# Optimization experiments

Measured on AMD Instinct MI355X. Metric: run time of the kernel, lower is better.

## Reference

```python
import jax, jax.numpy as jnp
import numpy as np
import math

B, S, D, H, L = 4, 2048, 512, 8, 2
HD = D // H
NG = (3, 4, 5)
V = 30000          # n_gram_vocab_size
BASE = 31          # rolling hash base
NPATCH = 16
PLEN = S // NPATCH


def _ln(x, w, b, eps):
    m = x.mean(-1, keepdims=True)
    v = ((x - m) ** 2).mean(-1, keepdims=True)
    return (x - m) * jax.lax.rsqrt(v + eps) * w + b


def setup_inputs() -> dict:
    key = jax.random.key(0)
    ks = jax.random.split(key, 16)

    def nrm(i, shape, std=0.02):
        return jax.random.normal(ks[i], shape, dtype=jnp.float32) * std

    return {
        "byte_seq": jax.random.randint(ks[0], (B, S), 0, 256, dtype=jnp.int32),
        "patch_boundaries": jnp.arange(NPATCH + 1, dtype=jnp.int32) * PLEN,
        "byte_emb": nrm(1, (256, D), 1.0 / math.sqrt(D)),
        "ng_emb": nrm(2, (len(NG), V, D)),
        "tl_qkv_w": nrm(3, (L, 3 * D, D)),
        "tl_qkv_b": jnp.zeros((L, 3 * D), jnp.float32),
        "tl_out_w": nrm(4, (L, D, D)),
        "tl_out_b": jnp.zeros((L, D), jnp.float32),
        "tl_ln1_w": jnp.ones((L, D), jnp.float32),
        "tl_ln1_b": jnp.zeros((L, D), jnp.float32),
        "tl_ln2_w": jnp.ones((L, D), jnp.float32),
        "tl_ln2_b": jnp.zeros((L, D), jnp.float32),
        "tl_ff1_w": nrm(5, (L, 4 * D, D)),
        "tl_ff1_b": jnp.zeros((L, 4 * D), jnp.float32),
        "tl_ff2_w": nrm(6, (L, D, 4 * D)),
        "tl_ff2_b": jnp.zeros((L, D), jnp.float32),
        "ca_qkv_w": nrm(7, (3 * D, D)),
        "ca_qkv_b": jnp.zeros((3 * D,), jnp.float32),
        "ca_out_w": nrm(8, (D, D)),
        "ca_out_b": jnp.zeros((D,), jnp.float32),
        "ca_ln_w": jnp.ones((D,), jnp.float32),
        "ca_ln_b": jnp.zeros((D,), jnp.float32),
        "norm_w": jnp.ones((D,), jnp.float32),
        "norm_b": jnp.zeros((D,), jnp.float32),
    }


def _forward(byte_seq, patch_boundaries, byte_emb, ng_emb,
             tl_qkv_w, tl_qkv_b, tl_out_w, tl_out_b,
             tl_ln1_w, tl_ln1_b, tl_ln2_w, tl_ln2_b,
             tl_ff1_w, tl_ff1_b, tl_ff2_w, tl_ff2_b,
             ca_qkv_w, ca_qkv_b, ca_out_w, ca_out_b, ca_ln_w, ca_ln_b,
             norm_w, norm_b):
    x = byte_emb[byte_seq]                                  # [B,S,D]

    # n-gram rolling hash == polynomial hash mod V; computed in parallel
    # as windowed dot products with modular base powers (exact same values
    # as the sequential rolling-update loop in the torch code).
    ng_scale = 1.0 / (len(NG) + 1)
    for idx, n in enumerate(NG):
        powers = jnp.array([pow(BASE, n - 1 - i, V) for i in range(n)],
                           dtype=byte_seq.dtype)
        windows = jnp.stack([byte_seq[:, j:S - n + 1 + j] for j in range(n)],
                            axis=-1)                        # [B,S-n+1,n]
        h = (windows * powers).sum(-1) % V                   # [B,S-n+1]
        x = x.at[:, n - 1:].add(ng_emb[idx][h] * ng_scale)

    scale = 1.0 / math.sqrt(HD)
    neg = jnp.where(jnp.triu(jnp.ones((S, S), dtype=bool), 1),
                    -jnp.inf, 0.0).astype(x.dtype)           # causal additive mask

    # post-norm TransformerEncoderLayer (relu activation, dropout=0/eval)
    for l in range(L):
        qkv = x @ tl_qkv_w[l].T + tl_qkv_b[l]                # [B,S,3D]
        q, k, v = jnp.split(qkv, 3, axis=-1)
        q = q.reshape(B, S, H, HD).transpose(0, 2, 1, 3)
        k = k.reshape(B, S, H, HD).transpose(0, 2, 1, 3)
        v = v.reshape(B, S, H, HD).transpose(0, 2, 1, 3)
        scores = jnp.einsum('bhqd,bhkd->bhqk', q, k) * scale + neg
        a = jax.nn.softmax(scores, axis=-1)
        o = jnp.einsum('bhqk,bhkd->bhqd', a, v).transpose(0, 2, 1, 3).reshape(B, S, D)
        o = o @ tl_out_w[l].T + tl_out_b[l]
        x = _ln(x + o, tl_ln1_w[l], tl_ln1_b[l], 1e-5)
        ff = jax.nn.relu(x @ tl_ff1_w[l].T + tl_ff1_b[l]) @ tl_ff2_w[l].T + tl_ff2_b[l]
        x = _ln(x + ff, tl_ln2_w[l], tl_ln2_b[l], 1e-5)

    # uniform patch boundaries -> vectorized patch cross-attention
    npatch = patch_boundaries.shape[0] - 1
    plen = S // npatch
    xp = x.reshape(B, npatch, plen, D)
    query = xp.mean(axis=2)                                  # [B,P,D]
    qn = _ln(query, ca_ln_w, ca_ln_b, 1e-6)
    kvn = _ln(xp, ca_ln_w, ca_ln_b, 1e-6)
    wq, wk, wv = jnp.split(ca_qkv_w, 3, axis=0)
    bq, bk, bv = jnp.split(ca_qkv_b, 3)
    q = (qn @ wq.T + bq).reshape(B, npatch, H, HD)
    k = (kvn @ wk.T + bk).reshape(B, npatch, plen, H, HD)
    v = (kvn @ wv.T + bv).reshape(B, npatch, plen, H, HD)
    s = jnp.einsum('bphd,bplhd->bphl', q, k) * scale
    a = jax.nn.softmax(s, axis=-1)
    o = jnp.einsum('bphl,bplhd->bphd', a, v).reshape(B, npatch, D)
    patches = query + (o @ ca_out_w.T + ca_out_b)

    return _ln(x, norm_w, norm_b, 1e-6), _ln(patches, norm_w, norm_b, 1e-6)


def reference(byte_seq, patch_boundaries, byte_emb, ng_emb,
              tl_qkv_w, tl_qkv_b, tl_out_w, tl_out_b,
              tl_ln1_w, tl_ln1_b, tl_ln2_w, tl_ln2_b,
              tl_ff1_w, tl_ff1_b, tl_ff2_w, tl_ff2_b,
              ca_qkv_w, ca_qkv_b, ca_out_w, ca_out_b, ca_ln_w, ca_ln_b,
              norm_w, norm_b):
    return _forward(byte_seq, patch_boundaries, byte_emb, ng_emb,
                    tl_qkv_w, tl_qkv_b, tl_out_w, tl_out_b,
                    tl_ln1_w, tl_ln1_b, tl_ln2_w, tl_ln2_b,
                    tl_ff1_w, tl_ff1_b, tl_ff2_w, tl_ff2_b,
                    ca_qkv_w, ca_qkv_b, ca_out_w, ca_out_b, ca_ln_w, ca_ln_b,
                    norm_w, norm_b)
```

## Files before the change

### kernel.cpp

```cpp
#include <hip/hip_runtime.h>
#include <hip/hip_bf16.h>

#define B_ 4
#define S_ 2048
#define D_ 512
#define H_ 8
#define HD_ 64
#define L_ 2
#define V_ 30000
#define NPATCH_ 16
#define PLEN_ 128

typedef short bf16x8 __attribute__((ext_vector_type(8)));
typedef float f32x4 __attribute__((ext_vector_type(4)));

__device__ __forceinline__ unsigned short f2bf(float f) {
    unsigned u = __float_as_uint(f);
    return (unsigned short)((u + 0x7FFFu + ((u >> 16) & 1u)) >> 16);
}

#define C0_ (2*1536*512/4)
#define C1_ (2*512*512/4)
#define C2_ (2*2048*512/4)
#define C3_ (2*512*2048/4)
#define C4_ (1024*512/4)
__global__ __launch_bounds__(256) void cast5_kernel(
    const float* __restrict__ s0, const float* __restrict__ s1,
    const float* __restrict__ s2, const float* __restrict__ s3,
    const float* __restrict__ s4,
    unsigned short* __restrict__ d0, unsigned short* __restrict__ d1,
    unsigned short* __restrict__ d2, unsigned short* __restrict__ d3,
    unsigned short* __restrict__ d4)
{
    int i = blockIdx.x * 256 + threadIdx.x;
    const float* s; unsigned short* d;
    if      (i < C0_)                  { s = s0; d = d0; }
    else if ((i -= C0_) < C1_)         { s = s1; d = d1; }
    else if ((i -= C1_) < C2_)         { s = s2; d = d2; }
    else if ((i -= C2_) < C3_)         { s = s3; d = d3; }
    else if ((i -= C3_) < C4_)         { s = s4; d = d4; }
    else return;
    const float4 v = *reinterpret_cast<const float4*>(s + (size_t)i * 4);
    ushort4 o;
    o.x = f2bf(v.x); o.y = f2bf(v.y); o.z = f2bf(v.z); o.w = f2bf(v.w);
    *reinterpret_cast<ushort4*>(d + (size_t)i * 4) = o;
}

__global__ __launch_bounds__(128) void embed_ngram_kernel(
    const int* __restrict__ bytes, const float* __restrict__ byte_emb,
    const float* __restrict__ ng_emb, float* __restrict__ x,
    unsigned short* __restrict__ xb)
{
    const int bs = blockIdx.x;
    const int s  = bs % S_;
    const int b  = bs / S_;
    const int d  = threadIdx.x * 4;
    const int* brow = bytes + (size_t)b * S_;

    const int c = brow[s];
    float4 v = *reinterpret_cast<const float4*>(byte_emb + (size_t)c * D_ + d);

    if (s >= 2) {
        int h = (brow[s-2]*961 + brow[s-1]*31 + brow[s]) % V_;
        const float4 g = *reinterpret_cast<const float4*>(ng_emb + ((size_t)0*V_ + h)*D_ + d);
        v.x += 0.25f*g.x; v.y += 0.25f*g.y; v.z += 0.25f*g.z; v.w += 0.25f*g.w;
    }
    if (s >= 3) {
        int h = (brow[s-3]*29791 + brow[s-2]*961 + brow[s-1]*31 + brow[s]) % V_;
        const float4 g = *reinterpret_cast<const float4*>(ng_emb + ((size_t)1*V_ + h)*D_ + d);
        v.x += 0.25f*g.x; v.y += 0.25f*g.y; v.z += 0.25f*g.z; v.w += 0.25f*g.w;
    }
    if (s >= 4) {
        int h = (brow[s-4]*23521 + brow[s-3]*29791 + brow[s-2]*961 + brow[s-1]*31 + brow[s]) % V_;
        const float4 g = *reinterpret_cast<const float4*>(ng_emb + ((size_t)2*V_ + h)*D_ + d);
        v.x += 0.25f*g.x; v.y += 0.25f*g.y; v.z += 0.25f*g.z; v.w += 0.25f*g.w;
    }
    *reinterpret_cast<float4*>(x + (size_t)bs * D_ + d) = v;
    ushort4 o;
    o.x = f2bf(v.x); o.y = f2bf(v.y); o.z = f2bf(v.z); o.w = f2bf(v.w);
    *reinterpret_cast<ushort4*>(xb + (size_t)bs * D_ + d) = o;
}

template<int DO_RELU, int BF16OUT, int BN>
__global__ __launch_bounds__(256) void mgemm_kernel(
    const unsigned short* __restrict__ Xb, const unsigned short* __restrict__ Wb,
    const float* __restrict__ bias, void* __restrict__ Yout,
    int M, int N, int K)
{
    constexpr int NT  = BN / 32;
    constexpr int NLB = BN / 32;
    __shared__ unsigned short As[128*64];
    __shared__ unsigned short Bs[BN*64];

    const int t    = threadIdx.x;
    const int lane = t & 63;
    const int w    = t >> 6;

    const int nwg = gridDim.x * gridDim.y;
    const int bid = blockIdx.y * gridDim.x + blockIdx.x;
    const int swz = (bid & 7) * (nwg >> 3) + (bid >> 3);
    const int bx  = swz % gridDim.x, by = swz / gridDim.x;

    const int bm   = by * 128, bn = bx * BN;
    const int l15  = lane & 15, lg = lane >> 4;
    const int wr   = w >> 1, wc = w & 1;

    int srow[4], scol[4];
#pragma unroll
    for (int i = 0; i < 4; ++i) {
        const int off = w*1024 + i*4096 + lane*16;
        srow[i] = off >> 7;
        scol[i] = ((off >> 4) & 7) ^ (srow[i] & 7);
    }

    f32x4 acc[4][NT];
#pragma unroll
    for (int mt = 0; mt < 4; ++mt)
#pragma unroll
        for (int nt = 0; nt < NT; ++nt) acc[mt][nt] = (f32x4){0.f,0.f,0.f,0.f};

    for (int kt = 0; kt < K; kt += 64) {
#pragma unroll
        for (int i = 0; i < 4; ++i) {
            const unsigned short* gA = Xb + (size_t)(bm + srow[i]) * K + kt + scol[i]*8;
            __builtin_amdgcn_global_load_lds(
                (const __attribute__((address_space(1))) void*)gA,
                (__attribute__((address_space(3))) void*)&As[w*512 + i*2048], 16, 0, 0);
        }
#pragma unroll
        for (int i = 0; i < NLB; ++i) {
            const unsigned short* gB = Wb + (size_t)(bn + srow[i]) * K + kt + scol[i]*8;
            __builtin_amdgcn_global_load_lds(
                (const __attribute__((address_space(1))) void*)gB,
                (__attribute__((address_space(3))) void*)&Bs[w*512 + i*2048], 16, 0, 0);
        }
        __syncthreads();

#pragma unroll
        for (int ks = 0; ks < 2; ++ks) {
            const int c16 = (ks*4 + lg) ^ (l15 & 7);
            bf16x8 a[4], b[NT];
#pragma unroll
            for (int mt = 0; mt < 4; ++mt)
                a[mt] = *reinterpret_cast<const bf16x8*>(&As[(wr*64 + mt*16 + l15)*64 + c16*8]);
#pragma unroll
            for (int nt = 0; nt < NT; ++nt)
                b[nt] = *reinterpret_cast<const bf16x8*>(&Bs[(wc*(BN/2) + nt*16 + l15)*64 + c16*8]);
#pragma unroll
            for (int mt = 0; mt < 4; ++mt)
#pragma unroll
                for (int nt = 0; nt < NT; ++nt)
                    acc[mt][nt] = __builtin_amdgcn_mfma_f32_16x16x32_bf16(
                        a[mt], b[nt], acc[mt][nt], 0, 0, 0);
        }
        __syncthreads();
    }

    float bv[NT];
#pragma unroll
    for (int nt = 0; nt < NT; ++nt) bv[nt] = bias[bn + wc*(BN/2) + nt*16 + l15];

#pragma unroll
    for (int mt = 0; mt < 4; ++mt) {
#pragma unroll
        for (int nt = 0; nt < NT; ++nt) {
            const int n = bn + wc*(BN/2) + nt*16 + l15;
#pragma unroll
            for (int r = 0; r < 4; ++r) {
                const int m = bm + wr*64 + mt*16 + 4*lg + r;
                float v = acc[mt][nt][r] + bv[nt];
                if (DO_RELU) v = fmaxf(v, 0.f);
                if (BF16OUT)
                    ((unsigned short*)Yout)[(size_t)m * N + n] = f2bf(v);
                else
                    ((float*)Yout)[(size_t)m * N + n] = v;
            }
        }
    }
}

__global__ __launch_bounds__(256) void attn_mfma_kernel(
    const unsigned short* __restrict__ qkvb, unsigned short* __restrict__ ob)
{
    __shared__ unsigned short Ks[128*72];
    __shared__ unsigned short Vt[64*136];
    __shared__ unsigned short Plds[4*16*136];

    const int t    = threadIdx.x;
    const int lane = t & 63;
    const int w    = t >> 6;
    const int qp   = blockIdx.x;
    const int bh   = blockIdx.y;
    const int h    = bh & 7;
    const int b    = bh >> 3;

    const unsigned short* base = qkvb + (size_t)b * S_ * 1536;
    const int l15 = lane & 15, lg = lane >> 4;
    const int skey = t >> 1;
    const int sd0  = (t & 1) * 32;
    const int scs  = (((skey >> 3) ^ ((t & 1) << 1)) << 3) + (skey & 7);
    unsigned short* pw_base = Plds + w*16*136;

    bf16x8 kr0, kr1, kr2, kr3, vr0, vr1, vr2, vr3;
#define LOADREG(KT) { \
        const unsigned short* p_ = base + (size_t)((KT) + skey) * 1536 + 512 + h*64 + sd0; \
        kr0 = *reinterpret_cast<const bf16x8*>(p_);       \
        kr1 = *reinterpret_cast<const bf16x8*>(p_ + 8);   \
        kr2 = *reinterpret_cast<const bf16x8*>(p_ + 16);  \
        kr3 = *reinterpret_cast<const bf16x8*>(p_ + 24);  \
        vr0 = *reinterpret_cast<const bf16x8*>(p_ + 512); \
        vr1 = *reinterpret_cast<const bf16x8*>(p_ + 520); \
        vr2 = *reinterpret_cast<const bf16x8*>(p_ + 528); \
        vr3 = *reinterpret_cast<const bf16x8*>(p_ + 536); }

    LOADREG(0);

#pragma unroll
    for (int half = 0; half < 2; ++half) {
        const int qb  = half ? (31 - qp) : qp;
        const int q0w = qb * 64 + w * 16;

        bf16x8 qf0, qf1;
        {
            const unsigned short* qr = base + (size_t)(q0w + l15) * 1536 + h*64 + lg*8;
            qf0 = *reinterpret_cast<const bf16x8*>(qr);
            qf1 = *reinterpret_cast<const bf16x8*>(qr + 32);
        }

        f32x4 oacc[4];
#pragma unroll
        for (int i = 0; i < 4; ++i) oacc[i] = (f32x4){0.f,0.f,0.f,0.f};
        float mrow[4] = {-INFINITY,-INFINITY,-INFINITY,-INFINITY};
        float lrow[4] = {0.f,0.f,0.f,0.f};

        const int ntiles = (qb + 2) >> 1;
        for (int tile = 0; tile < ntiles; ++tile) {
            const int kt = tile * 128;
            __syncthreads();
            *reinterpret_cast<bf16x8*>(&Ks[skey*72 + sd0])      = kr0;
            *reinterpret_cast<bf16x8*>(&Ks[skey*72 + sd0 + 8])  = kr1;
            *reinterpret_cast<bf16x8*>(&Ks[skey*72 + sd0 + 16]) = kr2;
            *reinterpret_cast<bf16x8*>(&Ks[skey*72 + sd0 + 24]) = kr3;
#pragma unroll
            for (int j = 0; j < 8; ++j) Vt[(sd0+j)*136    + scs] = (unsigned short)vr0[j];
#pragma unroll
            for (int j = 0; j < 8; ++j) Vt[(sd0+8+j)*136  + scs] = (unsigned short)vr1[j];
#pragma unroll
            for (int j = 0; j < 8; ++j) Vt[(sd0+16+j)*136 + scs] = (unsigned short)vr2[j];
#pragma unroll
            for (int j = 0; j < 8; ++j) Vt[(sd0+24+j)*136 + scs] = (unsigned short)vr3[j];
            __syncthreads();
            const int nkt = (tile + 1 < ntiles) ? (kt + 128) : 0;
            LOADREG(nkt);

            f32x4 sacc[8];
            __builtin_amdgcn_s_setprio(1);
#pragma unroll
            for (int kt16 = 0; kt16 < 8; ++kt16) {
                sacc[kt16] = (f32x4){0.f,0.f,0.f,0.f};
                const unsigned short* kp = &Ks[(kt16*16 + l15)*72 + lg*8];
                bf16x8 k0 = *reinterpret_cast<const bf16x8*>(kp);
                bf16x8 k1 = *reinterpret_cast<const bf16x8*>(kp + 32);
                sacc[kt16] = __builtin_amdgcn_mfma_f32_16x16x32_bf16(qf0, k0, sacc[kt16], 0, 0, 0);
                sacc[kt16] = __builtin_amdgcn_mfma_f32_16x16x32_bf16(qf1, k1, sacc[kt16], 0, 0, 0);
            }
            __builtin_amdgcn_s_setprio(0);

            const bool diag = (tile == ntiles - 1);
#pragma unroll
            for (int kt16 = 0; kt16 < 8; ++kt16) {
#pragma unroll
                for (int r = 0; r < 4; ++r) {
                    float s = sacc[kt16][r] * 0.125f;
                    if (diag) {
                        const int key = kt + kt16*16 + l15;
                        const int q   = q0w + 4*lg + r;
                        if (key > q) s = -INFINITY;
                    }
                    sacc[kt16][r] = s;
                }
            }
#pragma unroll
            for (int r = 0; r < 4; ++r) {
                float tm = fmaxf(
                    fmaxf(fmaxf(sacc[0][r], sacc[1][r]), fmaxf(sacc[2][r], sacc[3][r])),
                    fmaxf(fmaxf(sacc[4][r], sacc[5][r]), fmaxf(sacc[6][r], sacc[7][r])));
#pragma unroll
                for (int off = 8; off; off >>= 1) tm = fmaxf(tm, __shfl_xor(tm, off, 64));
                const float nm = fmaxf(mrow[r], tm);
                const float al = __expf(mrow[r] - nm);
                mrow[r] = nm;
                float ps = 0.f;
#pragma unroll
                for (int kt16 = 0; kt16 < 8; ++kt16) {
                    const float p = __expf(sacc[kt16][r] - nm);
                    ps += p;
                    pw_base[(4*lg + r)*136 + kt16*16 + l15] = f2bf(p);
                }
#pragma unroll
                for (int off = 8; off; off >>= 1) ps += __shfl_xor(ps, off, 64);
                lrow[r] = lrow[r]*al + ps;
#pragma unroll
                for (int dt = 0; dt < 4; ++dt) oacc[dt][r] *= al;
            }

            const unsigned short* pr = &pw_base[l15*136 + lg*8];
            bf16x8 pa0 = *reinterpret_cast<const bf16x8*>(pr);
            bf16x8 pa1 = *reinterpret_cast<const bf16x8*>(pr + 32);
            bf16x8 pa2 = *reinterpret_cast<const bf16x8*>(pr + 64);
            bf16x8 pa3 = *reinterpret_cast<const bf16x8*>(pr + 96);
            __builtin_amdgcn_s_setprio(1);
#pragma unroll
            for (int dt = 0; dt < 4; ++dt) {
                const unsigned short* vrow = &Vt[(dt*16 + l15)*136];
                bf16x8 v0 = *reinterpret_cast<const bf16x8*>(&vrow[(( 0 + lg) ^ (dt & 2))*8]);
                bf16x8 v1 = *reinterpret_cast<const bf16x8*>(&vrow[(( 4 + lg) ^ (dt & 2))*8]);
                bf16x8 v2 = *reinterpret_cast<const bf16x8*>(&vrow[(( 8 + lg) ^ (dt & 2))*8]);
                bf16x8 v3 = *reinterpret_cast<const bf16x8*>(&vrow[((12 + lg) ^ (dt & 2))*8]);
                oacc[dt] = __builtin_amdgcn_mfma_f32_16x16x32_bf16(pa0, v0, oacc[dt], 0, 0, 0);
                oacc[dt] = __builtin_amdgcn_mfma_f32_16x16x32_bf16(pa1, v1, oacc[dt], 0, 0, 0);
                oacc[dt] = __builtin_amdgcn_mfma_f32_16x16x32_bf16(pa2, v2, oacc[dt], 0, 0, 0);
                oacc[dt] = __builtin_amdgcn_mfma_f32_16x16x32_bf16(pa3, v3, oacc[dt], 0, 0, 0);
            }
            __builtin_amdgcn_s_setprio(0);
        }

#pragma unroll
        for (int dt = 0; dt < 4; ++dt) {
#pragma unroll
            for (int r = 0; r < 4; ++r) {
                const int q = q0w + 4*lg + r;
                ob[((size_t)b*S_ + q)*D_ + h*64 + dt*16 + l15] = f2bf(oacc[dt][r] / lrow[r]);
            }
        }
    }
#undef LOADREG
}

__global__ __launch_bounds__(256) void ln_kernel(
    float* __restrict__ dst, unsigned short* __restrict__ dst2,
    const float* __restrict__ src, const float* __restrict__ add,
    const float* __restrict__ w, const float* __restrict__ b, float eps)
{
    const int row = blockIdx.x, tid = threadIdx.x;
    const int lane = tid & 63, wave = tid >> 6;
    float2 v = *reinterpret_cast<const float2*>(src + (size_t)row * D_ + tid*2);
    if (add) {
        float2 a = *reinterpret_cast<const float2*>(add + (size_t)row * D_ + tid*2);
        v.x += a.x; v.y += a.y;
    }
    __shared__ float red[8];
    float s = v.x + v.y;
#pragma unroll
    for (int off = 32; off; off >>= 1) s += __shfl_xor(s, off, 64);
    if (lane == 0) red[wave] = s;
    __syncthreads();
    const float mean = (red[0]+red[1]+red[2]+red[3]) * (1.f/D_);
    const float d0 = v.x - mean, d1 = v.y - mean;
    float sq = d0*d0 + d1*d1;
#pragma unroll
    for (int off = 32; off; off >>= 1) sq += __shfl_xor(sq, off, 64);
    if (lane == 0) red[4+wave] = sq;
    __syncthreads();
    const float var = (red[4]+red[5]+red[6]+red[7]) * (1.f/D_);
    const float inv = rsqrtf(var + eps);
    const float o0 = d0*inv*w[tid*2] + b[tid*2];
    const float o1 = d1*inv*w[tid*2+1] + b[tid*2+1];
    if (dst)
        *reinterpret_cast<float2*>(dst + (size_t)row * D_ + tid*2) = make_float2(o0, o1);
    if (dst2) {
        ushort2 u; u.x = f2bf(o0); u.y = f2bf(o1);
        *reinterpret_cast<ushort2*>(dst2 + (size_t)row * D_ + tid*2) = u;
    }
}

__global__ __launch_bounds__(256) void patch_tail_kernel(
    const float* __restrict__ x, const float* __restrict__ kvf,
    const float* __restrict__ ca_qkv_w, const float* __restrict__ ca_qkv_b,
    const float* __restrict__ ca_out_w, const float* __restrict__ ca_out_b,
    const float* __restrict__ ca_ln_w, const float* __restrict__ ca_ln_b,
    const float* __restrict__ norm_w, const float* __restrict__ norm_b,
    float* __restrict__ out)
{
    __shared__ float query[512];
    __shared__ float qs[512];
    __shared__ float ps[8*128];
    __shared__ float os[512];
    __shared__ float red[64];
    __shared__ float mred[8], sred[8];

    const int t  = threadIdx.x;
    const int bp = blockIdx.x;
    const int d0 = t * 2;
    const int lane = t & 63, wave = t >> 6;

    {
        const float* base = x + (size_t)bp * PLEN_ * D_ + d0;
        float s0 = 0.f, s1 = 0.f;
        for (int l = 0; l < PLEN_; ++l) {
            float2 v = *reinterpret_cast<const float2*>(base + (size_t)l * D_);
            s0 += v.x; s1 += v.y;
        }
        query[d0] = s0 * (1.f/PLEN_);
        query[d0+1] = s1 * (1.f/PLEN_);
    }
    __syncthreads();

    float qv0 = query[d0], qv1 = query[d0+1];
    {
        float s = qv0 + qv1;
#pragma unroll
        for (int off = 32; off; off >>= 1) s += __shfl_xor(s, off, 64);
        if (lane == 0) red[wave] = s;
        __syncthreads();
        const float mean = (red[0]+red[1]+red[2]+red[3]) * (1.f/D_);
        const float e0 = qv0 - mean, e1 = qv1 - mean;
        float sq = e0*e0 + e1*e1;
#pragma unroll
        for (int off = 32; off; off >>= 1) sq += __shfl_xor(sq, off, 64);
        if (lane == 0) red[4+wave] = sq;
        __syncthreads();
        const float var = (red[4]+red[5]+red[6]+red[7]) * (1.f/D_);
        const float inv = rsqrtf(var + 1e-6f);
        qs[d0]   = e0*inv*ca_ln_w[d0]   + ca_ln_b[d0];
        qs[d0+1] = e1*inv*ca_ln_w[d0+1] + ca_ln_b[d0+1];
    }
    __syncthreads();

    float qp0, qp1;
    {
        const float* w0 = ca_qkv_w + (size_t)d0 * D_;
        float a0 = ca_qkv_b[d0], a1 = ca_qkv_b[d0+1];
        for (int e = 0; e < D_; e += 4) {
            const float4 qn4 = *reinterpret_cast<const float4*>(&qs[e]);
            const float4 wa = *reinterpret_cast<const float4*>(w0 + e);
            const float4 wb = *reinterpret_cast<const float4*>(w0 + D_ + e);
            a0 += qn4.x*wa.x + qn4.y*wa.y + qn4.z*wa.z + qn4.w*wa.w;
            a1 += qn4.x*wb.x + qn4.y*wb.y + qn4.z*wb.z + qn4.w*wb.w;
        }
        qp0 = a0 * 0.125f; qp1 = a1 * 0.125f;
    }
    __syncthreads();
    qs[d0] = qp0; qs[d0+1] = qp1;
    __syncthreads();

    {
        const int h = t >> 5, c = t & 31;
        const float* qh = &qs[h*64];
#pragma unroll
        for (int j = 0; j < 4; ++j) {
            const int l = c*4 + j;
            const float* krow = kvf + ((size_t)bp*PLEN_ + l)*1024 + h*64;
            float acc = 0.f;
            for (int e = 0; e < 64; e += 4) {
                const float4 qe = *reinterpret_cast<const float4*>(qh + e);
                const float4 ke = *reinterpret_cast<const float4*>(krow + e);
                acc += qe.x*ke.x + qe.y*ke.y + qe.z*ke.z + qe.w*ke.w;
            }
            ps[h*128 + l] = acc;
        }
    }
    __syncthreads();

    {
        const int h = t >> 5, c = t & 31;
        float m4 = fmaxf(fmaxf(ps[h*128+c*4], ps[h*128+c*4+1]),
                         fmaxf(ps[h*128+c*4+2], ps[h*128+c*4+3]));
        red[h*8 + (c>>2)] = 0.f;
        __syncthreads();
        float mt_ = m4;
#pragma unroll
        for (int off = 1; off < 4; off <<= 1) mt_ = fmaxf(mt_, __shfl_xor(mt_, off, 64));
        if ((c & 3) == 0) red[h*8 + (c>>2)] = mt_;
        __syncthreads();
        if (t < 8) {
            float m = red[t*8];
#pragma unroll
            for (int j = 1; j < 8; ++j) m = fmaxf(m, red[t*8+j]);
            mred[t] = m;
        }
        __syncthreads();
        const float mh = mred[h];
        float ssum = 0.f;
#pragma unroll
        for (int j = 0; j < 4; ++j) {
            const float p = __expf(ps[h*128 + c*4 + j] - mh);
            ps[h*128 + c*4 + j] = p;
            ssum += p;
        }
#pragma unroll
        for (int off = 1; off < 4; off <<= 1) ssum += __shfl_xor(ssum, off, 64);
        if ((c & 3) == 0) red[h*8 + (c>>2)] = ssum;
        __syncthreads();
        if (t < 8) {
            float s = 0.f;
#pragma unroll
            for (int j = 0; j < 8; ++j) s += red[t*8+j];
            sred[t] = 1.f / s;
        }
    }
    __syncthreads();

    {
        const int h = t >> 5;
        const float* vbase = kvf + (size_t)bp*PLEN_*1024 + 512 + d0;
        float a0 = 0.f, a1 = 0.f;
        const float* ph = &ps[h*128];
        for (int l = 0; l < PLEN_; ++l) {
            const float p = ph[l];
            const float2 vv = *reinterpret_cast<const float2*>(vbase + (size_t)l*1024);
            a0 += p * vv.x; a1 += p * vv.y;
        }
        os[d0]   = a0 * sred[h];
        os[d0+1] = a1 * sred[h];
    }
    __syncthreads();

    float r0, r1;
    {
        const float* w0 = ca_out_w + (size_t)d0 * D_;
        float a0 = ca_out_b[d0], a1 = ca_out_b[d0+1];
        for (int e = 0; e < D_; e += 4) {
            const float4 oe = *reinterpret_cast<const float4*>(&os[e]);
            const float4 wa = *reinterpret_cast<const float4*>(w0 + e);
            const float4 wb = *reinterpret_cast<const float4*>(w0 + D_ + e);
            a0 += oe.x*wa.x + oe.y*wa.y + oe.z*wa.z + oe.w*wa.w;
            a1 += oe.x*wb.x + oe.y*wb.y + oe.z*wb.z + oe.w*wb.w;
        }
        r0 = query[d0] + a0;
        r1 = query[d0+1] + a1;
    }
    {
        float s = r0 + r1;
#pragma unroll
        for (int off = 32; off; off >>= 1) s += __shfl_xor(s, off, 64);
        __syncthreads();
        if (lane == 0) red[wave] = s;
        __syncthreads();
        const float mean = (red[0]+red[1]+red[2]+red[3]) * (1.f/D_);
        const float e0 = r0 - mean, e1 = r1 - mean;
        float sq = e0*e0 + e1*e1;
#pragma unroll
        for (int off = 32; off; off >>= 1) sq += __shfl_xor(sq, off, 64);
        if (lane == 0) red[4+wave] = sq;
        __syncthreads();
        const float var = (red[4]+red[5]+red[6]+red[7]) * (1.f/D_);
        const float inv = rsqrtf(var + 1e-6f);
        float* orow = out + ((size_t)(B_*S_) + bp) * D_;
        orow[d0]   = e0*inv*norm_w[d0]   + norm_b[d0];
        orow[d0+1] = e1*inv*norm_w[d0+1] + norm_b[d0+1];
    }
}

extern "C" void kernel_launch(void* const* d_in, const int* in_sizes, int n_in,
                              void* d_out, int out_size, void* d_ws, size_t ws_size,
                              hipStream_t stream)
{
    const int*   byte_seq = (const int*)d_in[0];
    const float* byte_emb = (const float*)d_in[2];
    const float* ng_emb   = (const float*)d_in[3];
    const float* qkv_w = (const float*)d_in[4];
    const float* qkv_b = (const float*)d_in[5];
    const float* out_w = (const float*)d_in[6];
    const float* out_b = (const float*)d_in[7];
    const float* ln1_w = (const float*)d_in[8];
    const float* ln1_b = (const float*)d_in[9];
    const float* ln2_w = (const float*)d_in[10];
    const float* ln2_b = (const float*)d_in[11];
    const float* ff1_w = (const float*)d_in[12];
    const float* ff1_b = (const float*)d_in[13];
    const float* ff2_w = (const float*)d_in[14];
    const float* ff2_b = (const float*)d_in[15];
    const float* ca_qkv_w = (const float*)d_in[16];
    const float* ca_qkv_b = (const float*)d_in[17];
    const float* ca_out_w = (const float*)d_in[18];
    const float* ca_out_b = (const float*)d_in[19];
    const float* ca_ln_w  = (const float*)d_in[20];
    const float* ca_ln_b  = (const float*)d_in[21];
    const float* norm_w   = (const float*)d_in[22];
    const float* norm_b   = (const float*)d_in[23];
    float* out = (float*)d_out;

    char* ws = (char*)d_ws;
    const size_t MB = 1024*1024;
    float*          x     = (float*)(ws);
    char*           bufA  = ws + 16*MB;
    float*          bufB  = (float*)(ws + 48*MB);
    unsigned short* ob    = (unsigned short*)(ws + 64*MB);
    unsigned short* xb    = (unsigned short*)(ws + 72*MB);
    unsigned short* qkvw_b = (unsigned short*)(ws + 80*MB);
    unsigned short* outw_b = (unsigned short*)(ws + 83*MB);
    unsigned short* ff1w_b = (unsigned short*)(ws + 84*MB);
    unsigned short* ff2w_b = (unsigned short*)(ws + 88*MB);
    unsigned short* kvw_b  = (unsigned short*)(ws + 92*MB);

    unsigned short* qkvb = (unsigned short*)bufA;
    unsigned short* ff1b = (unsigned short*)bufA;
    float*          kvf  = (float*)bufA;

    const int M = B_ * S_;

    cast5_kernel<<<(C0_+C1_+C2_+C3_+C4_+255)/256, 256, 0, stream>>>(
        qkv_w, out_w, ff1_w, ff2_w, ca_qkv_w + 512*512,
        qkvw_b, outw_b, ff1w_b, ff2w_b, kvw_b);

    embed_ngram_kernel<<<M, 128, 0, stream>>>(byte_seq, byte_emb, ng_emb, x, xb);

    for (int l = 0; l < L_; ++l) {
        mgemm_kernel<0,1,128><<<dim3(1536/128, M/128), 256, 0, stream>>>(
            xb, qkvw_b + (size_t)l*1536*D_, qkv_b + l*1536, qkvb, M, 1536, D_);
        attn_mfma_kernel<<<dim3(S_/128, B_*H_), 256, 0, stream>>>(qkvb, ob);
        mgemm_kernel<0,0,64><<<dim3(D_/64, M/128), 256, 0, stream>>>(
            ob, outw_b + (size_t)l*D_*D_, out_b + l*D_, bufB, M, D_, D_);
        ln_kernel<<<M, 256, 0, stream>>>(x, xb, x, bufB, ln1_w + l*D_, ln1_b + l*D_, 1e-5f);
        mgemm_kernel<1,1,128><<<dim3(2048/128, M/128), 256, 0, stream>>>(
            xb, ff1w_b + (size_t)l*2048*D_, ff1_b + l*2048, ff1b, M, 2048, D_);
        mgemm_kernel<0,0,64><<<dim3(D_/64, M/128), 256, 0, stream>>>(
            ff1b, ff2w_b + (size_t)l*D_*2048, ff2_b + l*D_, bufB, M, D_, 2048);
        ln_kernel<<<M, 256, 0, stream>>>(x, xb, x, bufB, ln2_w + l*D_, ln2_b + l*D_, 1e-5f);
    }

    ln_kernel<<<M, 256, 0, stream>>>(nullptr, xb, x, nullptr, ca_ln_w, ca_ln_b, 1e-6f);
    mgemm_kernel<0,0,128><<<dim3(1024/128, M/128), 256, 0, stream>>>(
        xb, kvw_b, ca_qkv_b + 512, kvf, M, 1024, D_);
    patch_tail_kernel<<<B_*NPATCH_, 256, 0, stream>>>(
        x, kvf, ca_qkv_w, ca_qkv_b, ca_out_w, ca_out_b,
        ca_ln_w, ca_ln_b, norm_w, norm_b, out);

    ln_kernel<<<M, 256, 0, stream>>>(out, nullptr, x, nullptr, norm_w, norm_b, 1e-6f);
}
```

Measured before the change: 513.4 us.

## Write V transposed from QKV GEMM epilogue and drop LDS transpose in attention

The QKV GEMM epilogue now writes Q and K into a 1024-wide buffer and V transposed (per batch, dim-major over sequence) into a separate buffer. The attention kernel can then store V into LDS with vector writes instead of scalar transposing stores. The P tile in LDS also gets an XOR swizzle to reduce bank conflicts. In exchange, the GEMM's V stores are strided scattered 2-byte writes, which may be poorly coalesced.

```diff
diff --git a/kernel.cpp b/kernel.cpp
--- a/kernel.cpp
+++ b/kernel.cpp
@@ -81,11 +81,11 @@
     *reinterpret_cast<ushort4*>(xb + (size_t)bs * D_ + d) = o;
 }
 
-template<int DO_RELU, int BF16OUT, int BN>
+template<int DO_RELU, int BF16OUT, int BN, int VT>
 __global__ __launch_bounds__(256) void mgemm_kernel(
     const unsigned short* __restrict__ Xb, const unsigned short* __restrict__ Wb,
     const float* __restrict__ bias, void* __restrict__ Yout,
-    int M, int N, int K)
+    unsigned short* __restrict__ vtb, int M, int N, int K)
 {
     constexpr int NT  = BN / 32;
     constexpr int NLB = BN / 32;
@@ -170,17 +170,24 @@
                 const int m = bm + wr*64 + mt*16 + 4*lg + r;
                 float v = acc[mt][nt][r] + bv[nt];
                 if (DO_RELU) v = fmaxf(v, 0.f);
-                if (BF16OUT)
+                if constexpr (VT) {
+                    if (n < 1024)
+                        ((unsigned short*)Yout)[(size_t)m * 1024 + n] = f2bf(v);
+                    else
+                        vtb[((size_t)(m >> 11) * 512 + (n - 1024)) * 2048 + (m & 2047)] = f2bf(v);
+                } else if constexpr (BF16OUT) {
                     ((unsigned short*)Yout)[(size_t)m * N + n] = f2bf(v);
-                else
+                } else {
                     ((float*)Yout)[(size_t)m * N + n] = v;
+                }
             }
         }
     }
 }
 
 __global__ __launch_bounds__(256) void attn_mfma_kernel(
-    const unsigned short* __restrict__ qkvb, unsigned short* __restrict__ ob)
+    const unsigned short* __restrict__ qkvb, const unsigned short* __restrict__ vtb,
+    unsigned short* __restrict__ ob)
 {
     __shared__ unsigned short Ks[128*72];
     __shared__ unsigned short Vt[64*136];
@@ -194,24 +201,28 @@
     const int h    = bh & 7;
     const int b    = bh >> 3;
 
-    const unsigned short* base = qkvb + (size_t)b * S_ * 1536;
+    const unsigned short* base = qkvb + (size_t)b * S_ * 1024;
     const int l15 = lane & 15, lg = lane >> 4;
     const int skey = t >> 1;
     const int sd0  = (t & 1) * 32;
-    const int scs  = (((skey >> 3) ^ ((t & 1) << 1)) << 3) + (skey & 7);
+    const int sdv  = t >> 2;
+    const int skc  = (t & 3) * 32;
+    const unsigned short* vbase = vtb + ((size_t)b * 512 + h*64 + sdv) * 2048;
     unsigned short* pw_base = Plds + w*16*136;
+    const int pxor = ((l15 >> 3) & 1) << 1;
 
     bf16x8 kr0, kr1, kr2, kr3, vr0, vr1, vr2, vr3;
 #define LOADREG(KT) { \
-        const unsigned short* p_ = base + (size_t)((KT) + skey) * 1536 + 512 + h*64 + sd0; \
-        kr0 = *reinterpret_cast<const bf16x8*>(p_);       \
-        kr1 = *reinterpret_cast<const bf16x8*>(p_ + 8);   \
-        kr2 = *reinterpret_cast<const bf16x8*>(p_ + 16);  \
-        kr3 = *reinterpret_cast<const bf16x8*>(p_ + 24);  \
-        vr0 = *reinterpret_cast<const bf16x8*>(p_ + 512); \
-        vr1 = *reinterpret_cast<const bf16x8*>(p_ + 520); \
-        vr2 = *reinterpret_cast<const bf16x8*>(p_ + 528); \
-        vr3 = *reinterpret_cast<const bf16x8*>(p_ + 536); }
+        const unsigned short* pk_ = base + (size_t)((KT) + skey) * 1024 + 512 + h*64 + sd0; \
+        kr0 = *reinterpret_cast<const bf16x8*>(pk_);       \
+        kr1 = *reinterpret_cast<const bf16x8*>(pk_ + 8);   \
+        kr2 = *reinterpret_cast<const bf16x8*>(pk_ + 16);  \
+        kr3 = *reinterpret_cast<const bf16x8*>(pk_ + 24);  \
+        const unsigned short* pv_ = vbase + (KT) + skc;    \
+        vr0 = *reinterpret_cast<const bf16x8*>(pv_);       \
+        vr1 = *reinterpret_cast<const bf16x8*>(pv_ + 8);   \
+        vr2 = *reinterpret_cast<const bf16x8*>(pv_ + 16);  \
+        vr3 = *reinterpret_cast<const bf16x8*>(pv_ + 24); }
 
     LOADREG(0);
 
@@ -222,7 +233,7 @@
 
         bf16x8 qf0, qf1;
         {
-            const unsigned short* qr = base + (size_t)(q0w + l15) * 1536 + h*64 + lg*8;
+            const unsigned short* qr = base + (size_t)(q0w + l15) * 1024 + h*64 + lg*8;
             qf0 = *reinterpret_cast<const bf16x8*>(qr);
             qf1 = *reinterpret_cast<const bf16x8*>(qr + 32);
         }
@@ -241,14 +252,10 @@
             *reinterpret_cast<bf16x8*>(&Ks[skey*72 + sd0 + 8])  = kr1;
             *reinterpret_cast<bf16x8*>(&Ks[skey*72 + sd0 + 16]) = kr2;
             *reinterpret_cast<bf16x8*>(&Ks[skey*72 + sd0 + 24]) = kr3;
-#pragma unroll
-            for (int j = 0; j < 8; ++j) Vt[(sd0+j)*136    + scs] = (unsigned short)vr0[j];
-#pragma unroll
-            for (int j = 0; j < 8; ++j) Vt[(sd0+8+j)*136  + scs] = (unsigned short)vr1[j];
-#pragma unroll
-            for (int j = 0; j < 8; ++j) Vt[(sd0+16+j)*136 + scs] = (unsigned short)vr2[j];
-#pragma unroll
-            for (int j = 0; j < 8; ++j) Vt[(sd0+24+j)*136 + scs] = (unsigned short)vr3[j];
+            *reinterpret_cast<bf16x8*>(&Vt[sdv*136 + skc])      = vr0;
+            *reinterpret_cast<bf16x8*>(&Vt[sdv*136 + skc + 8])  = vr1;
+            *reinterpret_cast<bf16x8*>(&Vt[sdv*136 + skc + 16]) = vr2;
+            *reinterpret_cast<bf16x8*>(&Vt[sdv*136 + skc + 24]) = vr3;
             __syncthreads();
             const int nkt = (tile + 1 < ntiles) ? (kt + 128) : 0;
             LOADREG(nkt);
@@ -291,11 +298,13 @@
                 const float al = __expf(mrow[r] - nm);
                 mrow[r] = nm;
                 float ps = 0.f;
+                const int prow = (4*lg + r)*136;
+                const int cswz = ((lg & 2) << 3);
 #pragma unroll
                 for (int kt16 = 0; kt16 < 8; ++kt16) {
                     const float p = __expf(sacc[kt16][r] - nm);
                     ps += p;
-                    pw_base[(4*lg + r)*136 + kt16*16 + l15] = f2bf(p);
+                    pw_base[prow + ((kt16*16 + l15) ^ cswz)] = f2bf(p);
                 }
 #pragma unroll
                 for (int off = 8; off; off >>= 1) ps += __shfl_xor(ps, off, 64);
@@ -304,19 +313,19 @@
                 for (int dt = 0; dt < 4; ++dt) oacc[dt][r] *= al;
             }
 
-            const unsigned short* pr = &pw_base[l15*136 + lg*8];
-            bf16x8 pa0 = *reinterpret_cast<const bf16x8*>(pr);
-            bf16x8 pa1 = *reinterpret_cast<const bf16x8*>(pr + 32);
-            bf16x8 pa2 = *reinterpret_cast<const bf16x8*>(pr + 64);
-            bf16x8 pa3 = *reinterpret_cast<const bf16x8*>(pr + 96);
+            const unsigned short* pr = &pw_base[l15*136];
+            bf16x8 pa0 = *reinterpret_cast<const bf16x8*>(&pr[(( 0 + lg) ^ pxor)*8]);
+            bf16x8 pa1 = *reinterpret_cast<const bf16x8*>(&pr[(( 4 + lg) ^ pxor)*8]);
+            bf16x8 pa2 = *reinterpret_cast<const bf16x8*>(&pr[(( 8 + lg) ^ pxor)*8]);
+            bf16x8 pa3 = *reinterpret_cast<const bf16x8*>(&pr[((12 + lg) ^ pxor)*8]);
             __builtin_amdgcn_s_setprio(1);
 #pragma unroll
             for (int dt = 0; dt < 4; ++dt) {
                 const unsigned short* vrow = &Vt[(dt*16 + l15)*136];
-                bf16x8 v0 = *reinterpret_cast<const bf16x8*>(&vrow[(( 0 + lg) ^ (dt & 2))*8]);
-                bf16x8 v1 = *reinterpret_cast<const bf16x8*>(&vrow[(( 4 + lg) ^ (dt & 2))*8]);
-                bf16x8 v2 = *reinterpret_cast<const bf16x8*>(&vrow[(( 8 + lg) ^ (dt & 2))*8]);
-                bf16x8 v3 = *reinterpret_cast<const bf16x8*>(&vrow[((12 + lg) ^ (dt & 2))*8]);
+                bf16x8 v0 = *reinterpret_cast<const bf16x8*>(&vrow[( 0 + lg)*8]);
+                bf16x8 v1 = *reinterpret_cast<const bf16x8*>(&vrow[( 4 + lg)*8]);
+                bf16x8 v2 = *reinterpret_cast<const bf16x8*>(&vrow[( 8 + lg)*8]);
+                bf16x8 v3 = *reinterpret_cast<const bf16x8*>(&vrow[(12 + lg)*8]);
                 oacc[dt] = __builtin_amdgcn_mfma_f32_16x16x32_bf16(pa0, v0, oacc[dt], 0, 0, 0);
                 oacc[dt] = __builtin_amdgcn_mfma_f32_16x16x32_bf16(pa1, v1, oacc[dt], 0, 0, 0);
                 oacc[dt] = __builtin_amdgcn_mfma_f32_16x16x32_bf16(pa2, v2, oacc[dt], 0, 0, 0);
@@ -586,6 +595,7 @@
     float*          x     = (float*)(ws);
     char*           bufA  = ws + 16*MB;
     float*          bufB  = (float*)(ws + 48*MB);
+    unsigned short* vtb   = (unsigned short*)(ws + 48*MB);
     unsigned short* ob    = (unsigned short*)(ws + 64*MB);
     unsigned short* xb    = (unsigned short*)(ws + 72*MB);
     unsigned short* qkvw_b = (unsigned short*)(ws + 80*MB);
@@ -607,22 +617,22 @@
     embed_ngram_kernel<<<M, 128, 0, stream>>>(byte_seq, byte_emb, ng_emb, x, xb);
 
     for (int l = 0; l < L_; ++l) {
-        mgemm_kernel<0,1,128><<<dim3(1536/128, M/128), 256, 0, stream>>>(
-            xb, qkvw_b + (size_t)l*1536*D_, qkv_b + l*1536, qkvb, M, 1536, D_);
-        attn_mfma_kernel<<<dim3(S_/128, B_*H_), 256, 0, stream>>>(qkvb, ob);
-        mgemm_kernel<0,0,64><<<dim3(D_/64, M/128), 256, 0, stream>>>(
-            ob, outw_b + (size_t)l*D_*D_, out_b + l*D_, bufB, M, D_, D_);
+        mgemm_kernel<0,1,128,1><<<dim3(1536/128, M/128), 256, 0, stream>>>(
+            xb, qkvw_b + (size_t)l*1536*D_, qkv_b + l*1536, qkvb, vtb, M, 1536, D_);
+        attn_mfma_kernel<<<dim3(S_/128, B_*H_), 256, 0, stream>>>(qkvb, vtb, ob);
+        mgemm_kernel<0,0,64,0><<<dim3(D_/64, M/128), 256, 0, stream>>>(
+            ob, outw_b + (size_t)l*D_*D_, out_b + l*D_, bufB, nullptr, M, D_, D_);
         ln_kernel<<<M, 256, 0, stream>>>(x, xb, x, bufB, ln1_w + l*D_, ln1_b + l*D_, 1e-5f);
-        mgemm_kernel<1,1,128><<<dim3(2048/128, M/128), 256, 0, stream>>>(
-            xb, ff1w_b + (size_t)l*2048*D_, ff1_b + l*2048, ff1b, M, 2048, D_);
-        mgemm_kernel<0,0,64><<<dim3(D_/64, M/128), 256, 0, stream>>>(
-            ff1b, ff2w_b + (size_t)l*D_*2048, ff2_b + l*D_, bufB, M, D_, 2048);
+        mgemm_kernel<1,1,128,0><<<dim3(2048/128, M/128), 256, 0, stream>>>(
+            xb, ff1w_b + (size_t)l*2048*D_, ff1_b + l*2048, ff1b, nullptr, M, 2048, D_);
+        mgemm_kernel<0,0,64,0><<<dim3(D_/64, M/128), 256, 0, stream>>>(
+            ff1b, ff2w_b + (size_t)l*D_*2048, ff2_b + l*D_, bufB, nullptr, M, D_, 2048);
         ln_kernel<<<M, 256, 0, stream>>>(x, xb, x, bufB, ln2_w + l*D_, ln2_b + l*D_, 1e-5f);
     }
 
     ln_kernel<<<M, 256, 0, stream>>>(nullptr, xb, x, nullptr, ca_ln_w, ca_ln_b, 1e-6f);
-    mgemm_kernel<0,0,128><<<dim3(1024/128, M/128), 256, 0, stream>>>(
-        xb, kvw_b, ca_qkv_b + 512, kvf, M, 1024, D_);
+    mgemm_kernel<0,0,128,0><<<dim3(1024/128, M/128), 256, 0, stream>>>(
+        xb, kvw_b, ca_qkv_b + 512, kvf, nullptr, M, 1024, D_);
     patch_tail_kernel<<<B_*NPATCH_, 256, 0, stream>>>(
         x, kvf, ca_qkv_w, ca_qkv_b, ca_out_w, ca_out_b,
         ca_ln_w, ca_ln_b, norm_w, norm_b, out);
```

Result: faster. 502.4 us (-2.1%).
